# Kernel optimization log

Measured on AMD Instinct MI355X. Metric: run time of the kernel, lower is better.

Reference implementation:

```python
import jax, jax.numpy as jnp
import numpy as np
import math

N_CTX = 2048
D = 1024
N_HEAD = 16
B = 4
D_FF = 4 * D

def gelu(x):
    return 0.5 * x * (1 + jnp.tanh(jnp.sqrt(2 / jnp.pi) * (x + 0.044715 * x ** 3)))

def layer_norm(x, g, b, e=1e-5):
    u = x.mean(-1, keepdims=True)
    s = ((x - u) ** 2).mean(-1, keepdims=True)
    return g * (x - u) / jnp.sqrt(s + e) + b

def setup_inputs() -> dict:
    key = jax.random.key(0)
    ks = jax.random.split(key, 6)
    std = 0.02
    return {
        "x": jax.random.normal(ks[0], (B, N_CTX, D), dtype=jnp.float32),
        "w_attn": jax.random.normal(ks[1], (D, 3 * D), dtype=jnp.float32) * std,
        "b_attn": jnp.zeros((3 * D,), jnp.float32),
        "w_aproj": jax.random.normal(ks[2], (D, D), dtype=jnp.float32) * std,
        "b_aproj": jnp.zeros((D,), jnp.float32),
        "g1": jnp.ones((D,), jnp.float32),
        "b1": jnp.zeros((D,), jnp.float32),
        "w_fc": jax.random.normal(ks[3], (D, D_FF), dtype=jnp.float32) * std,
        "b_fc": jnp.zeros((D_FF,), jnp.float32),
        "w_mproj": jax.random.normal(ks[4], (D_FF, D), dtype=jnp.float32) * std,
        "b_mproj": jnp.zeros((D,), jnp.float32),
        "g2": jnp.ones((D,), jnp.float32),
        "b2": jnp.zeros((D,), jnp.float32),
    }

def reference(x, w_attn, b_attn, w_aproj, b_aproj, g1, b1, w_fc, b_fc, w_mproj, b_mproj, g2, b2):
    Bz, S, _ = x.shape
    hd = D // N_HEAD
    # qkv projection (Conv1D = addmm)
    qkv = x @ w_attn + b_attn  # [B,S,3D]
    q, k, v = jnp.split(qkv, 3, axis=-1)
    # split heads -> [B,H,S,hd]
    q = q.reshape(Bz, S, N_HEAD, hd).transpose(0, 2, 1, 3)
    k = k.reshape(Bz, S, N_HEAD, hd).transpose(0, 2, 1, 3)
    v = v.reshape(Bz, S, N_HEAD, hd).transpose(0, 2, 1, 3)
    w = jnp.einsum('bhqd,bhkd->bhqk', q, k) / math.sqrt(hd)  # scale=True
    mask = jnp.tril(jnp.ones((S, S), jnp.float32))[None, None]
    w = w * mask - 1e9 * (1 - mask)
    w = jax.nn.softmax(w, axis=-1)
    a = jnp.einsum('bhqk,bhkd->bhqd', w, v)
    a = a.transpose(0, 2, 1, 3).reshape(Bz, S, D)  # merge heads
    a = a @ w_aproj + b_aproj
    n = layer_norm(x + a, g1, b1)
    h = gelu(n @ w_fc + b_fc)
    m = h @ w_mproj + b_mproj
    return layer_norm(n + m, g2, b2)
```

## Files before the change

### kernel.cpp

```cpp
#include <hip/hip_runtime.h>
#include <math.h>

#define S_CTX 2048
#define DMODEL 1024
#define NHEAD 16
#define HD 64
#define BATCH 4
#define DFF 4096

typedef __bf16 bf16x8 __attribute__((ext_vector_type(8)));
typedef float f32x4 __attribute__((ext_vector_type(4)));

__device__ __forceinline__ unsigned short f2bf(float f) {
    union { float f; unsigned int u; } v; v.f = f;
    unsigned int u = v.u;
    u += 0x7fffu + ((u >> 16) & 1u);
    return (unsigned short)(u >> 16);
}

__device__ __forceinline__ float gelu_f(float v) {
    const float c = 0.7978845608028654f;
    float u = c * (v + 0.044715f * v * v * v);
    return 0.5f * v * (1.0f + tanhf(u));
}

#define GLOAD16(gsrc, ldst)                                                     \
    __builtin_amdgcn_global_load_lds(                                           \
        (const __attribute__((address_space(1))) void*)(gsrc),                  \
        (__attribute__((address_space(3))) void*)(ldst), 16, 0, 0)

__global__ __launch_bounds__(256)
void wcast_kernel(const float* __restrict__ W, short* __restrict__ WT, int K, int N)
{
    __shared__ float tile[32][33];
    const int n0 = blockIdx.x * 32;
    const int k0 = blockIdx.y * 32;
    {
        const int r  = threadIdx.x >> 3;
        const int c4 = (threadIdx.x & 7) * 4;
        const float4 v = *(const float4*)&W[(size_t)(k0 + r) * N + n0 + c4];
        tile[r][c4 + 0] = v.x; tile[r][c4 + 1] = v.y;
        tile[r][c4 + 2] = v.z; tile[r][c4 + 3] = v.w;
    }
    __syncthreads();
    const int n  = threadIdx.x >> 3;
    const int k4 = (threadIdx.x & 7) * 4;
    ushort4 o = make_ushort4(f2bf(tile[k4 + 0][n]), f2bf(tile[k4 + 1][n]),
                             f2bf(tile[k4 + 2][n]), f2bf(tile[k4 + 3][n]));
    *(ushort4*)&WT[(size_t)(n0 + n) * K + k0 + k4] = o;
}

__global__ __launch_bounds__(256)
void cast_act_kernel(const float* __restrict__ in, short* __restrict__ out, int n4)
{
    int idx = blockIdx.x * blockDim.x + threadIdx.x;
    const int stride = gridDim.x * blockDim.x;
    for (; idx < n4; idx += stride) {
        const float4 v = ((const float4*)in)[idx];
        ((ushort4*)out)[idx] = make_ushort4(f2bf(v.x), f2bf(v.y), f2bf(v.z), f2bf(v.w));
    }
}

template<int GELU, int OBF16>
__global__ __launch_bounds__(256)
void mfma_gemm_kernel(const short* __restrict__ Ab, const short* __restrict__ BTb,
                      const float* __restrict__ bias, void* __restrict__ Cout,
                      int M, int N, int K)
{
    __shared__ short As[128 * 32];
    __shared__ short Bs[128 * 32];

    const int tid  = threadIdx.x;
    const int lane = tid & 63;
    const int wave = tid >> 6;
    const int wr   = (wave >> 1) * 64;
    const int wc   = (wave & 1) * 64;
    const int m0   = blockIdx.y * 128;
    const int n0   = blockIdx.x * 128;

    const int lrow = tid >> 2;
    const int slot = tid & 3;
    const int sw   = slot ^ (lrow & 3);
    const short* Ag0 = Ab  + (size_t)(m0 + lrow) * K      + sw * 8;
    const short* Ag1 = Ab  + (size_t)(m0 + 64 + lrow) * K + sw * 8;
    const short* Bg0 = BTb + (size_t)(n0 + lrow) * K      + sw * 8;
    const short* Bg1 = BTb + (size_t)(n0 + 64 + lrow) * K + sw * 8;

    short* AsW = As + wave * 512;
    short* BsW = Bs + wave * 512;

    f32x4 acc[4][4];
    #pragma unroll
    for (int i = 0; i < 4; ++i)
        #pragma unroll
        for (int j = 0; j < 4; ++j) acc[i][j] = (f32x4){0.f, 0.f, 0.f, 0.f};

    const int r  = lane & 15;
    const int kg = lane >> 4;
    int aoff[4], boff[4];
    #pragma unroll
    for (int m = 0; m < 4; ++m) {
        const int arow = wr + m * 16 + r;
        aoff[m] = arow * 32 + (kg ^ (arow & 3)) * 8;
        const int bcol = wc + m * 16 + r;
        boff[m] = bcol * 32 + (kg ^ (bcol & 3)) * 8;
    }

    for (int k0 = 0; k0 < K; k0 += 32) {
        __syncthreads();
        GLOAD16(Ag0 + k0, AsW);
        GLOAD16(Ag1 + k0, AsW + 2048);
        GLOAD16(Bg0 + k0, BsW);
        GLOAD16(Bg1 + k0, BsW + 2048);
        __syncthreads();

        bf16x8 af[4], bfr[4];
        #pragma unroll
        for (int m = 0; m < 4; ++m) af[m]  = *(const bf16x8*)(As + aoff[m]);
        #pragma unroll
        for (int n = 0; n < 4; ++n) bfr[n] = *(const bf16x8*)(Bs + boff[n]);
        #pragma unroll
        for (int m = 0; m < 4; ++m)
            #pragma unroll
            for (int n = 0; n < 4; ++n)
                acc[m][n] = __builtin_amdgcn_mfma_f32_16x16x32_bf16(
                    af[m], bfr[n], acc[m][n], 0, 0, 0);
    }

    const int crow0 = m0 + wr + kg * 4;
    const int ccol0 = n0 + wc + r;
    #pragma unroll
    for (int m = 0; m < 4; ++m) {
        #pragma unroll
        for (int i = 0; i < 4; ++i) {
            const size_t row = (size_t)(crow0 + m * 16 + i);
            #pragma unroll
            for (int n = 0; n < 4; ++n) {
                float v = acc[m][n][i] + bias[ccol0 + n * 16];
                if (GELU) v = gelu_f(v);
                if (OBF16) ((short*)Cout)[row * N + ccol0 + n * 16] = (short)f2bf(v);
                else       ((float*)Cout)[row * N + ccol0 + n * 16] = v;
            }
        }
    }
}

__global__ __launch_bounds__(256)
void attn_mfma_kernel(const short* __restrict__ qkvb, short* __restrict__ out)
{
    __shared__ short Qs[64 * 64];
    __shared__ short Ks[64 * 64];
    __shared__ short Vt[64 * 64];
    __shared__ short Pl[4][16 * 72];

    const int tid  = threadIdx.x;
    const int lane = tid & 63;
    const int wave = tid >> 6;
    const int qt = blockIdx.x, h = blockIdx.y, b = blockIdx.z;
    const int q0 = qt * 64;

    const int r  = lane & 15;
    const int kg = lane >> 4;
    const size_t rstr = 3 * DMODEL;

    {
        const short* qbase = qkvb + ((size_t)(b * S_CTX + q0)) * rstr + h * HD;
        #pragma unroll
        for (int rr = 0; rr < 2; ++rr) {
            const int rl = wave * 16 + rr * 8 + (lane >> 3);
            const int sl = lane & 7;
            GLOAD16(qbase + (size_t)rl * rstr + ((sl ^ (rl & 7)) * 8),
                    Qs + wave * 1024 + rr * 512);
        }
    }

    float m_i[4], l_i[4];
    f32x4 o[4];
    #pragma unroll
    for (int i = 0; i < 4; ++i) {
        m_i[i] = -1e30f; l_i[i] = 0.0f;
        o[i] = (f32x4){0.f, 0.f, 0.f, 0.f};
    }

    for (int kt = 0; kt <= qt; ++kt) {
        const int k0 = kt * 64;
        __syncthreads();

        {
            const short* kbase = qkvb + ((size_t)(b * S_CTX + k0)) * rstr + DMODEL + h * HD;
            #pragma unroll
            for (int rr = 0; rr < 2; ++rr) {
                const int rl = wave * 16 + rr * 8 + (lane >> 3);
                const int sl = lane & 7;
                GLOAD16(kbase + (size_t)rl * rstr + ((sl ^ (rl & 7)) * 8),
                        Ks + wave * 1024 + rr * 512);
            }
        }
        {
            const int d0 = (tid & 15) * 4;
            const int kb = (tid >> 4) * 4;
            const short* vsrc = qkvb + ((size_t)(b * S_CTX + k0 + kb)) * rstr
                                + 2 * DMODEL + h * HD + d0;
            const ushort4 r0 = *(const ushort4*)(vsrc);
            const ushort4 r1 = *(const ushort4*)(vsrc + rstr);
            const ushort4 r2 = *(const ushort4*)(vsrc + 2 * rstr);
            const ushort4 r3 = *(const ushort4*)(vsrc + 3 * rstr);
            const unsigned short e0[4] = {r0.x, r0.y, r0.z, r0.w};
            const unsigned short e1[4] = {r1.x, r1.y, r1.z, r1.w};
            const unsigned short e2[4] = {r2.x, r2.y, r2.z, r2.w};
            const unsigned short e3[4] = {r3.x, r3.y, r3.z, r3.w};
            #pragma unroll
            for (int dd = 0; dd < 4; ++dd) {
                const int d = d0 + dd;
                const int byteoff = d * 128 + (((kb >> 3) ^ (d & 7)) * 16) + ((kb & 4) * 2);
                *(ushort4*)((char*)Vt + byteoff) = make_ushort4(e0[dd], e1[dd], e2[dd], e3[dd]);
            }
        }
        __syncthreads();

        f32x4 s4[4];
        #pragma unroll
        for (int c = 0; c < 4; ++c) s4[c] = (f32x4){0.f, 0.f, 0.f, 0.f};
        #pragma unroll
        for (int kb2 = 0; kb2 < 2; ++kb2) {
            const int qrow = wave * 16 + r;
            const bf16x8 af = *(const bf16x8*)(Qs + qrow * 64 +
                                (((kb2 * 4 + kg) ^ (qrow & 7)) * 8));
            #pragma unroll
            for (int c = 0; c < 4; ++c) {
                const int krow = c * 16 + r;
                const bf16x8 bfv = *(const bf16x8*)(Ks + krow * 64 +
                                    (((kb2 * 4 + kg) ^ (krow & 7)) * 8));
                s4[c] = __builtin_amdgcn_mfma_f32_16x16x32_bf16(af, bfv, s4[c], 0, 0, 0);
            }
        }

        const int rowg0 = q0 + wave * 16 + kg * 4;
        #pragma unroll
        for (int reg = 0; reg < 4; ++reg) {
            float sv[4];
            #pragma unroll
            for (int c = 0; c < 4; ++c) {
                const int colg = k0 + c * 16 + r;
                const float v = s4[c][reg] * 0.125f;
                sv[c] = (colg <= rowg0 + reg) ? v : -1e30f;
            }
            float rmax = fmaxf(fmaxf(sv[0], sv[1]), fmaxf(sv[2], sv[3]));
            rmax = fmaxf(rmax, __shfl_xor(rmax, 1));
            rmax = fmaxf(rmax, __shfl_xor(rmax, 2));
            rmax = fmaxf(rmax, __shfl_xor(rmax, 4));
            rmax = fmaxf(rmax, __shfl_xor(rmax, 8));
            const float mnew = fmaxf(m_i[reg], rmax);
            const float sc   = __expf(m_i[reg] - mnew);
            float rs = 0.0f;
            #pragma unroll
            for (int c = 0; c < 4; ++c) {
                const float pc = __expf(sv[c] - mnew);
                rs += pc;
                Pl[wave][(kg * 4 + reg) * 72 + c * 16 + r] = (short)f2bf(pc);
            }
            rs += __shfl_xor(rs, 1);
            rs += __shfl_xor(rs, 2);
            rs += __shfl_xor(rs, 4);
            rs += __shfl_xor(rs, 8);
            l_i[reg] = l_i[reg] * sc + rs;
            m_i[reg] = mnew;
            #pragma unroll
            for (int db = 0; db < 4; ++db) o[db][reg] *= sc;
        }

        #pragma unroll
        for (int kb2 = 0; kb2 < 2; ++kb2) {
            const bf16x8 pa = *(const bf16x8*)(&Pl[wave][r * 72 + kb2 * 32 + kg * 8]);
            #pragma unroll
            for (int db = 0; db < 4; ++db) {
                const int drow = db * 16 + r;
                const bf16x8 bv = *(const bf16x8*)(Vt + drow * 64 +
                                    (((kb2 * 4 + kg) ^ (drow & 7)) * 8));
                o[db] = __builtin_amdgcn_mfma_f32_16x16x32_bf16(pa, bv, o[db], 0, 0, 0);
            }
        }
    }

    #pragma unroll
    for (int reg = 0; reg < 4; ++reg) {
        const float inv = 1.0f / l_i[reg];
        const size_t rowg = (size_t)(b * S_CTX) + q0 + wave * 16 + kg * 4 + reg;
        #pragma unroll
        for (int db = 0; db < 4; ++db)
            out[rowg * DMODEL + h * HD + db * 16 + r] = (short)f2bf(o[db][reg] * inv);
    }
}

template<int WB>
__global__ __launch_bounds__(256)
void ln_res_kernel(const float* __restrict__ in1, const float* __restrict__ in2,
                   const float* __restrict__ g, const float* __restrict__ bb,
                   float* __restrict__ out, short* __restrict__ ob)
{
    const int row = blockIdx.x;
    const int tid = threadIdx.x;
    const size_t base = (size_t)row * DMODEL + tid * 4;

    const float4 x1 = *(const float4*)(in1 + base);
    const float4 x2 = *(const float4*)(in2 + base);
    const float y0 = x1.x + x2.x, y1 = x1.y + x2.y;
    const float y2 = x1.z + x2.z, y3 = x1.w + x2.w;

    float s1 = y0 + y1 + y2 + y3;
    float s2 = y0 * y0 + y1 * y1 + y2 * y2 + y3 * y3;
    #pragma unroll
    for (int off = 1; off < 64; off <<= 1) {
        s1 += __shfl_xor(s1, off);
        s2 += __shfl_xor(s2, off);
    }
    __shared__ float red[8];
    if ((tid & 63) == 0) {
        red[tid >> 6]       = s1;
        red[4 + (tid >> 6)] = s2;
    }
    __syncthreads();
    s1 = red[0] + red[1] + red[2] + red[3];
    s2 = red[4] + red[5] + red[6] + red[7];

    const float mean = s1 * (1.0f / DMODEL);
    const float var  = s2 * (1.0f / DMODEL) - mean * mean;
    const float rstd = rsqrtf(var + 1e-5f);

    const float4 g4 = *(const float4*)(g + tid * 4);
    const float4 b4 = *(const float4*)(bb + tid * 4);
    float4 o;
    o.x = g4.x * ((y0 - mean) * rstd) + b4.x;
    o.y = g4.y * ((y1 - mean) * rstd) + b4.y;
    o.z = g4.z * ((y2 - mean) * rstd) + b4.z;
    o.w = g4.w * ((y3 - mean) * rstd) + b4.w;
    *(float4*)(out + base) = o;
    if (WB)
        *(ushort4*)(ob + base) = make_ushort4(f2bf(o.x), f2bf(o.y), f2bf(o.z), f2bf(o.w));
}

extern "C" void kernel_launch(void* const* d_in, const int* in_sizes, int n_in,
                              void* d_out, int out_size, void* d_ws, size_t ws_size,
                              hipStream_t stream)
{
    const float* x       = (const float*)d_in[0];
    const float* w_attn  = (const float*)d_in[1];
    const float* b_attn  = (const float*)d_in[2];
    const float* w_aproj = (const float*)d_in[3];
    const float* b_aproj = (const float*)d_in[4];
    const float* g1      = (const float*)d_in[5];
    const float* b1      = (const float*)d_in[6];
    const float* w_fc    = (const float*)d_in[7];
    const float* b_fc    = (const float*)d_in[8];
    const float* w_mproj = (const float*)d_in[9];
    const float* b_mproj = (const float*)d_in[10];
    const float* g2      = (const float*)d_in[11];
    const float* b2      = (const float*)d_in[12];
    float* outp = (float*)d_out;

    char* wsb = (char*)d_ws;
    short* qkvb = (short*)wsb;
    short* hb   = (short*)wsb;
    short* nb   = (short*)(wsb + (size_t)(64u << 20));
    float* t    = (float*)(wsb + (size_t)(80u << 20));
    short* wT_attn  = (short*)(wsb + (size_t)(112u << 20));
    short* wT_aproj = wT_attn + 3145728;
    short* wT_fc    = wT_aproj + 1048576;
    short* wT_mproj = wT_fc + 4194304;
    short* xb = (short*)d_out;
    short* ab = (short*)d_out;

    const int M = BATCH * S_CTX;

    wcast_kernel<<<dim3(3 * DMODEL / 32, DMODEL / 32), 256, 0, stream>>>(w_attn, wT_attn, DMODEL, 3 * DMODEL);
    wcast_kernel<<<dim3(DMODEL / 32, DMODEL / 32), 256, 0, stream>>>(w_aproj, wT_aproj, DMODEL, DMODEL);
    wcast_kernel<<<dim3(DFF / 32, DMODEL / 32), 256, 0, stream>>>(w_fc, wT_fc, DMODEL, DFF);
    wcast_kernel<<<dim3(DMODEL / 32, DFF / 32), 256, 0, stream>>>(w_mproj, wT_mproj, DFF, DMODEL);
    cast_act_kernel<<<2048, 256, 0, stream>>>(x, xb, M * DMODEL / 4);

    mfma_gemm_kernel<0, 1><<<dim3(3 * DMODEL / 128, M / 128), 256, 0, stream>>>(
        xb, wT_attn, b_attn, (void*)qkvb, M, 3 * DMODEL, DMODEL);

    attn_mfma_kernel<<<dim3(S_CTX / 64, NHEAD, BATCH), 256, 0, stream>>>(qkvb, ab);

    mfma_gemm_kernel<0, 0><<<dim3(DMODEL / 128, M / 128), 256, 0, stream>>>(
        ab, wT_aproj, b_aproj, (void*)t, M, DMODEL, DMODEL);

    ln_res_kernel<1><<<M, 256, 0, stream>>>(x, t, g1, b1, outp, nb);

    mfma_gemm_kernel<1, 1><<<dim3(DFF / 128, M / 128), 256, 0, stream>>>(
        nb, wT_fc, b_fc, (void*)hb, M, DFF, DMODEL);

    mfma_gemm_kernel<0, 0><<<dim3(DMODEL / 128, M / 128), 256, 0, stream>>>(
        hb, wT_mproj, b_mproj, (void*)t, M, DMODEL, DFF);

    ln_res_kernel<0><<<M, 256, 0, stream>>>(outp, t, g2, b2, outp, nullptr);
}
```

Baseline: 769.0 us.

## Restructure causal attention: 128-row Q tiles, paired blocks, double-buffered K/V

The attention kernel now handles 128 query rows per block, with each wave owning 32 rows held in registers. Each block processes a pair of query tiles (pairidx and 15-pairidx) so causal work is balanced across blocks. K and V tiles are double-buffered in LDS: the next tile is prefetched while the current one is computed, and setprio hints raise wave priority around the MFMA sections. The goal is better K/V reuse, latency hiding and load balance, in exchange for more registers and LDS per block and a smaller grid of 512 blocks.

```diff
diff --git a/kernel.cpp b/kernel.cpp
--- a/kernel.cpp
+++ b/kernel.cpp
@@ -148,147 +148,196 @@
 __global__ __launch_bounds__(256)
 void attn_mfma_kernel(const short* __restrict__ qkvb, short* __restrict__ out)
 {
-    __shared__ short Qs[64 * 64];
-    __shared__ short Ks[64 * 64];
-    __shared__ short Vt[64 * 64];
-    __shared__ short Pl[4][16 * 72];
+    __shared__ short Ks[2][64 * 64];
+    __shared__ short Vt[2][64 * 64];
+    __shared__ short Pl[4][32 * 72];
 
     const int tid  = threadIdx.x;
     const int lane = tid & 63;
     const int wave = tid >> 6;
-    const int qt = blockIdx.x, h = blockIdx.y, b = blockIdx.z;
-    const int q0 = qt * 64;
-
+    const int pairidx = blockIdx.x;
+    const int h = blockIdx.y, b = blockIdx.z;
     const int r  = lane & 15;
     const int kg = lane >> 4;
-    const size_t rstr = 3 * DMODEL;
-
-    {
-        const short* qbase = qkvb + ((size_t)(b * S_CTX + q0)) * rstr + h * HD;
-        #pragma unroll
-        for (int rr = 0; rr < 2; ++rr) {
-            const int rl = wave * 16 + rr * 8 + (lane >> 3);
-            const int sl = lane & 7;
-            GLOAD16(qbase + (size_t)rl * rstr + ((sl ^ (rl & 7)) * 8),
-                    Qs + wave * 1024 + rr * 512);
-        }
-    }
-
-    float m_i[4], l_i[4];
-    f32x4 o[4];
-    #pragma unroll
-    for (int i = 0; i < 4; ++i) {
-        m_i[i] = -1e30f; l_i[i] = 0.0f;
-        o[i] = (f32x4){0.f, 0.f, 0.f, 0.f};
-    }
-
-    for (int kt = 0; kt <= qt; ++kt) {
-        const int k0 = kt * 64;
-        __syncthreads();
+    const size_t rstr  = 3 * DMODEL;
+    const size_t bbase = (size_t)b * S_CTX;
+
+    const int vd0 = (tid & 15) * 4;
+    const int vkb = (tid >> 4) * 4;
+    const short* vbase = qkvb + (bbase + vkb) * rstr + 2 * DMODEL + h * HD + vd0;
+    const int krl0 = wave * 8 + (lane >> 3);
+    const int ksl  = lane & 7;
+    const short* kbase0 = qkvb + bbase * rstr + DMODEL + h * HD;
+
+    for (int half = 0; half < 2; ++half) {
+        const int qt = half ? (15 - pairidx) : pairidx;
+        const int q0 = qt * 128;
+        const int nkt = 2 * qt + 2;
+
+        bf16x8 qf[2][2];
+        #pragma unroll
+        for (int m = 0; m < 2; ++m)
+            #pragma unroll
+            for (int kb2 = 0; kb2 < 2; ++kb2)
+                qf[m][kb2] = *(const bf16x8*)(qkvb
+                    + (bbase + q0 + wave * 32 + m * 16 + r) * rstr
+                    + h * HD + kb2 * 32 + kg * 8);
+
+        float m_i[2][4], l_i[2][4];
+        f32x4 o[2][4];
+        #pragma unroll
+        for (int m = 0; m < 2; ++m)
+            #pragma unroll
+            for (int i = 0; i < 4; ++i) {
+                m_i[m][i] = -1e30f; l_i[m][i] = 0.0f;
+                o[m][i] = (f32x4){0.f, 0.f, 0.f, 0.f};
+            }
 
         {
-            const short* kbase = qkvb + ((size_t)(b * S_CTX + k0)) * rstr + DMODEL + h * HD;
             #pragma unroll
             for (int rr = 0; rr < 2; ++rr) {
-                const int rl = wave * 16 + rr * 8 + (lane >> 3);
-                const int sl = lane & 7;
-                GLOAD16(kbase + (size_t)rl * rstr + ((sl ^ (rl & 7)) * 8),
-                        Ks + wave * 1024 + rr * 512);
-            }
-        }
-        {
-            const int d0 = (tid & 15) * 4;
-            const int kb = (tid >> 4) * 4;
-            const short* vsrc = qkvb + ((size_t)(b * S_CTX + k0 + kb)) * rstr
-                                + 2 * DMODEL + h * HD + d0;
-            const ushort4 r0 = *(const ushort4*)(vsrc);
-            const ushort4 r1 = *(const ushort4*)(vsrc + rstr);
-            const ushort4 r2 = *(const ushort4*)(vsrc + 2 * rstr);
-            const ushort4 r3 = *(const ushort4*)(vsrc + 3 * rstr);
-            const unsigned short e0[4] = {r0.x, r0.y, r0.z, r0.w};
-            const unsigned short e1[4] = {r1.x, r1.y, r1.z, r1.w};
-            const unsigned short e2[4] = {r2.x, r2.y, r2.z, r2.w};
-            const unsigned short e3[4] = {r3.x, r3.y, r3.z, r3.w};
+                const int rl = rr * 32 + krl0;
+                GLOAD16(kbase0 + (size_t)rl * rstr + ((ksl ^ (rl & 7)) * 8),
+                        &Ks[0][(rr * 32 + wave * 8) * 64]);
+            }
+            ushort4 vr[4];
+            #pragma unroll
+            for (int j = 0; j < 4; ++j)
+                vr[j] = *(const ushort4*)(vbase + (size_t)j * rstr);
+            const unsigned short* vp = (const unsigned short*)vr;
             #pragma unroll
             for (int dd = 0; dd < 4; ++dd) {
-                const int d = d0 + dd;
-                const int byteoff = d * 128 + (((kb >> 3) ^ (d & 7)) * 16) + ((kb & 4) * 2);
-                *(ushort4*)((char*)Vt + byteoff) = make_ushort4(e0[dd], e1[dd], e2[dd], e3[dd]);
+                const int d  = vd0 + dd;
+                const int up = (vkb >> 2) ^ (((d >> 2) & 3) << 2);
+                *(ushort4*)((char*)&Vt[0][0] + d * 128 + up * 8) =
+                    make_ushort4(vp[0 + dd], vp[4 + dd], vp[8 + dd], vp[12 + dd]);
             }
         }
         __syncthreads();
 
-        f32x4 s4[4];
-        #pragma unroll
-        for (int c = 0; c < 4; ++c) s4[c] = (f32x4){0.f, 0.f, 0.f, 0.f};
-        #pragma unroll
-        for (int kb2 = 0; kb2 < 2; ++kb2) {
-            const int qrow = wave * 16 + r;
-            const bf16x8 af = *(const bf16x8*)(Qs + qrow * 64 +
-                                (((kb2 * 4 + kg) ^ (qrow & 7)) * 8));
-            #pragma unroll
-            for (int c = 0; c < 4; ++c) {
-                const int krow = c * 16 + r;
-                const bf16x8 bfv = *(const bf16x8*)(Ks + krow * 64 +
-                                    (((kb2 * 4 + kg) ^ (krow & 7)) * 8));
-                s4[c] = __builtin_amdgcn_mfma_f32_16x16x32_bf16(af, bfv, s4[c], 0, 0, 0);
-            }
+        for (int t = 0; t < nkt; ++t) {
+            const int cur = t & 1;
+            const bool pre = (t + 1 < nkt);
+            ushort4 vr[4];
+            if (pre) {
+                const int k0n = (t + 1) * 64;
+                #pragma unroll
+                for (int rr = 0; rr < 2; ++rr) {
+                    const int rl = rr * 32 + krl0;
+                    GLOAD16(kbase0 + (size_t)(k0n + rl) * rstr + ((ksl ^ (rl & 7)) * 8),
+                            &Ks[cur ^ 1][(rr * 32 + wave * 8) * 64]);
+                }
+                #pragma unroll
+                for (int j = 0; j < 4; ++j)
+                    vr[j] = *(const ushort4*)(vbase + (size_t)(k0n + j) * rstr);
+            }
+
+            f32x4 s4[2][4];
+            #pragma unroll
+            for (int m = 0; m < 2; ++m)
+                #pragma unroll
+                for (int c = 0; c < 4; ++c) s4[m][c] = (f32x4){0.f, 0.f, 0.f, 0.f};
+            __builtin_amdgcn_s_setprio(1);
+            #pragma unroll
+            for (int kb2 = 0; kb2 < 2; ++kb2) {
+                #pragma unroll
+                for (int c = 0; c < 4; ++c) {
+                    const int krow = c * 16 + r;
+                    const bf16x8 kf = *(const bf16x8*)(&Ks[cur][0]
+                        + krow * 64 + (((kb2 * 4 + kg) ^ (krow & 7)) * 8));
+                    #pragma unroll
+                    for (int m = 0; m < 2; ++m)
+                        s4[m][c] = __builtin_amdgcn_mfma_f32_16x16x32_bf16(
+                            qf[m][kb2], kf, s4[m][c], 0, 0, 0);
+                }
+            }
+            __builtin_amdgcn_s_setprio(0);
+
+            const int k0 = t * 64;
+            #pragma unroll
+            for (int m = 0; m < 2; ++m) {
+                const int rowg0 = q0 + wave * 32 + m * 16 + kg * 4;
+                #pragma unroll
+                for (int reg = 0; reg < 4; ++reg) {
+                    float sv[4];
+                    #pragma unroll
+                    for (int c = 0; c < 4; ++c) {
+                        const int colg = k0 + c * 16 + r;
+                        const float v = s4[m][c][reg] * 0.125f;
+                        sv[c] = (colg <= rowg0 + reg) ? v : -1e30f;
+                    }
+                    float rmax = fmaxf(fmaxf(sv[0], sv[1]), fmaxf(sv[2], sv[3]));
+                    rmax = fmaxf(rmax, __shfl_xor(rmax, 1));
+                    rmax = fmaxf(rmax, __shfl_xor(rmax, 2));
+                    rmax = fmaxf(rmax, __shfl_xor(rmax, 4));
+                    rmax = fmaxf(rmax, __shfl_xor(rmax, 8));
+                    const float mnew = fmaxf(m_i[m][reg], rmax);
+                    const float sc   = __expf(m_i[m][reg] - mnew);
+                    float rs = 0.0f;
+                    #pragma unroll
+                    for (int c = 0; c < 4; ++c) {
+                        const float pc = __expf(sv[c] - mnew);
+                        rs += pc;
+                        Pl[wave][(m * 16 + kg * 4 + reg) * 72 + c * 16 + r] =
+                            (short)f2bf(pc);
+                    }
+                    rs += __shfl_xor(rs, 1);
+                    rs += __shfl_xor(rs, 2);
+                    rs += __shfl_xor(rs, 4);
+                    rs += __shfl_xor(rs, 8);
+                    l_i[m][reg] = l_i[m][reg] * sc + rs;
+                    m_i[m][reg] = mnew;
+                    #pragma unroll
+                    for (int db = 0; db < 4; ++db) o[m][db][reg] *= sc;
+                }
+            }
+
+            __builtin_amdgcn_s_setprio(1);
+            #pragma unroll
+            for (int kb2 = 0; kb2 < 2; ++kb2) {
+                bf16x8 pa[2];
+                #pragma unroll
+                for (int m = 0; m < 2; ++m)
+                    pa[m] = *(const bf16x8*)(&Pl[wave][(m * 16 + r) * 72
+                                                       + kb2 * 32 + kg * 8]);
+                #pragma unroll
+                for (int db = 0; db < 4; ++db) {
+                    const int drow = db * 16 + r;
+                    const bf16x8 bv = *(const bf16x8*)(&Vt[cur][0]
+                        + drow * 64 + (((kb2 * 4 + kg) ^ (((drow >> 2) & 3) << 1)) * 8));
+                    #pragma unroll
+                    for (int m = 0; m < 2; ++m)
+                        o[m][db] = __builtin_amdgcn_mfma_f32_16x16x32_bf16(
+                            pa[m], bv, o[m][db], 0, 0, 0);
+                }
+            }
+            __builtin_amdgcn_s_setprio(0);
+
+            if (pre) {
+                const unsigned short* vp = (const unsigned short*)vr;
+                #pragma unroll
+                for (int dd = 0; dd < 4; ++dd) {
+                    const int d  = vd0 + dd;
+                    const int up = (vkb >> 2) ^ (((d >> 2) & 3) << 2);
+                    *(ushort4*)((char*)&Vt[cur ^ 1][0] + d * 128 + up * 8) =
+                        make_ushort4(vp[0 + dd], vp[4 + dd], vp[8 + dd], vp[12 + dd]);
+                }
+            }
+            __syncthreads();
         }
 
-        const int rowg0 = q0 + wave * 16 + kg * 4;
-        #pragma unroll
-        for (int reg = 0; reg < 4; ++reg) {
-            float sv[4];
-            #pragma unroll
-            for (int c = 0; c < 4; ++c) {
-                const int colg = k0 + c * 16 + r;
-                const float v = s4[c][reg] * 0.125f;
-                sv[c] = (colg <= rowg0 + reg) ? v : -1e30f;
-            }
-            float rmax = fmaxf(fmaxf(sv[0], sv[1]), fmaxf(sv[2], sv[3]));
-            rmax = fmaxf(rmax, __shfl_xor(rmax, 1));
-            rmax = fmaxf(rmax, __shfl_xor(rmax, 2));
-            rmax = fmaxf(rmax, __shfl_xor(rmax, 4));
-            rmax = fmaxf(rmax, __shfl_xor(rmax, 8));
-            const float mnew = fmaxf(m_i[reg], rmax);
-            const float sc   = __expf(m_i[reg] - mnew);
-            float rs = 0.0f;
-            #pragma unroll
-            for (int c = 0; c < 4; ++c) {
-                const float pc = __expf(sv[c] - mnew);
-                rs += pc;
-                Pl[wave][(kg * 4 + reg) * 72 + c * 16 + r] = (short)f2bf(pc);
-            }
-            rs += __shfl_xor(rs, 1);
-            rs += __shfl_xor(rs, 2);
-            rs += __shfl_xor(rs, 4);
-            rs += __shfl_xor(rs, 8);
-            l_i[reg] = l_i[reg] * sc + rs;
-            m_i[reg] = mnew;
-            #pragma unroll
-            for (int db = 0; db < 4; ++db) o[db][reg] *= sc;
+        #pragma unroll
+        for (int m = 0; m < 2; ++m) {
+            #pragma unroll
+            for (int reg = 0; reg < 4; ++reg) {
+                const float inv = 1.0f / l_i[m][reg];
+                const size_t rowg = bbase + q0 + wave * 32 + m * 16 + kg * 4 + reg;
+                #pragma unroll
+                for (int db = 0; db < 4; ++db)
+                    out[rowg * DMODEL + h * HD + db * 16 + r] =
+                        (short)f2bf(o[m][db][reg] * inv);
+            }
         }
-
-        #pragma unroll
-        for (int kb2 = 0; kb2 < 2; ++kb2) {
-            const bf16x8 pa = *(const bf16x8*)(&Pl[wave][r * 72 + kb2 * 32 + kg * 8]);
-            #pragma unroll
-            for (int db = 0; db < 4; ++db) {
-                const int drow = db * 16 + r;
-                const bf16x8 bv = *(const bf16x8*)(Vt + drow * 64 +
-                                    (((kb2 * 4 + kg) ^ (drow & 7)) * 8));
-                o[db] = __builtin_amdgcn_mfma_f32_16x16x32_bf16(pa, bv, o[db], 0, 0, 0);
-            }
-        }
-    }
-
-    #pragma unroll
-    for (int reg = 0; reg < 4; ++reg) {
-        const float inv = 1.0f / l_i[reg];
-        const size_t rowg = (size_t)(b * S_CTX) + q0 + wave * 16 + kg * 4 + reg;
-        #pragma unroll
-        for (int db = 0; db < 4; ++db)
-            out[rowg * DMODEL + h * HD + db * 16 + r] = (short)f2bf(o[db][reg] * inv);
     }
 }
 
@@ -381,7 +430,7 @@
     mfma_gemm_kernel<0, 1><<<dim3(3 * DMODEL / 128, M / 128), 256, 0, stream>>>(
         xb, wT_attn, b_attn, (void*)qkvb, M, 3 * DMODEL, DMODEL);
 
-    attn_mfma_kernel<<<dim3(S_CTX / 64, NHEAD, BATCH), 256, 0, stream>>>(qkvb, ab);
+    attn_mfma_kernel<<<dim3(8, NHEAD, BATCH), 256, 0, stream>>>(qkvb, ab);
 
     mfma_gemm_kernel<0, 0><<<dim3(DMODEL / 128, M / 128), 256, 0, stream>>>(
         ab, wT_aproj, b_aproj, (void*)t, M, DMODEL, DMODEL);
```

Measured after the change: 639.8 us. 16.8% less time.
